# Optimization experiments

Hardware: AMD Instinct MI355X
Metric: run time of the kernel (lower is better)

The kernel has to match this reference:

```python
import jax, jax.numpy as jnp
import numpy as np
from jax import lax

E = 1e-13            # WENO smoothness epsilon
MULT_BIAS = 0.1      # weno5_mult_bias
PADS = (2, 2, 0, 0, 1, 0)


def _conv1d(x, w, b, pad):
    # x: [1, Cin, N], w: [Cout, Cin, K], b: [Cout]
    y = lax.conv_general_dilated(x, w, window_strides=(1,), padding=[(pad, pad)],
                                 dimension_numbers=('NCH', 'OIH', 'NCH'))
    return y + b[None, :, None]


def _cnn(dif, params):
    # inner_nn_weno5: 5 Conv+ELU blocks then Conv+Sigmoid; dif: [N]
    x = dif[None, None, :]
    for i in range(6):
        x = _conv1d(x, params[2 * i], params[2 * i + 1], PADS[i])
        x = jax.nn.elu(x) if i < 5 else jax.nn.sigmoid(x)
    return x[0, 0]  # [N]


def _avg_diff(uu):
    # __get_average_diff: average of left/right forward differences, edges replicated
    d = uu[1:] - uu[:-1]                       # [N-1]
    d_left = jnp.concatenate([d, d[-1:]])      # [N]
    d_right = jnp.concatenate([d[:1], d])      # [N]
    return 0.5 * (d_left + d_right)


def _weno5(uu, params):
    # w5_minus=True, mweno=True, mapped=False, trainable=True
    def fluxes(u):
        um, umm = jnp.roll(u, 1), jnp.roll(u, 2)
        up, upp = jnp.roll(u, -1), jnp.roll(u, -2)
        f0 = (11 * u - 7 * up + 2 * upp) / 6
        f1 = (2 * um + 5 * u - up) / 6
        f2 = (-umm + 5 * um + 2 * u) / 6
        return f0, f1, f2

    def betas(u):
        um, umm = jnp.roll(u, 1), jnp.roll(u, 2)
        up, upp = jnp.roll(u, -1), jnp.roll(u, -2)
        b0 = 13 / 12 * (u - 2 * up + upp) ** 2 + 0.25 * (3 * u - 4 * up + upp) ** 2
        b1 = 13 / 12 * (um - 2 * u + up) ** 2 + 0.25 * (um - up) ** 2
        b2 = 13 / 12 * (umm - 2 * um + u) ** 2 + 0.25 * (umm - 4 * um + 3 * u) ** 2
        return b0, b1, b2

    u_right = jnp.roll(uu, -1)
    fp = fluxes(u_right)
    fn = fluxes(uu)
    bp = list(betas(u_right))
    bn = list(betas(uu))

    # trainable beta correction from the small CNN flux limiter
    bm = _cnn(_avg_diff(uu), params) + MULT_BIAS
    bp = [b * jnp.roll(bm, k - 1) for k, b in enumerate(bp)]
    bn = [b * jnp.roll(bm, k - 1) for k, b in enumerate(bn)]

    ds = (0.1, 0.6, 0.3)

    def omegas(bs):  # mweno=True variant, then normalize
        brs = (bs[2] - bs[0]) ** 2
        om = [d / (E + b) ** 2 * (brs + (E + b) ** 2) for b, d in zip(bs, ds)]
        s = om[0] + om[1] + om[2]
        return [o / s for o in om]

    op = omegas(bp)
    on = omegas(bn)
    fluxp = op[0] * fp[0] + op[1] * fp[1] + op[2] * fp[2]
    fluxn = on[0] * fn[0] + on[1] * fn[1] + on[2] * fn[2]
    return fluxp - fluxn


def setup_inputs() -> dict:
    key = jax.random.key(0)
    ks = jax.random.split(key, 13)
    N = 2097152
    uu = jax.random.normal(ks[0], (N,), dtype=jnp.float32)
    shapes = [(20, 1, 5), (40, 20, 5), (80, 40, 1), (40, 80, 1), (20, 40, 3), (1, 20, 1)]
    inp = {'uu': uu}
    for i, (co, ci, k) in enumerate(shapes):
        fan_in = ci * k
        scale = jnp.float32(1.0 / np.sqrt(fan_in))
        inp[f'w{i + 1}'] = jax.random.normal(ks[2 * i + 1], (co, ci, k), dtype=jnp.float32) * scale
        inp[f'b{i + 1}'] = jax.random.normal(ks[2 * i + 2], (co,), dtype=jnp.float32) * 0.01
    return inp


def reference(uu, w1, b1, w2, b2, w3, b3, w4, b4, w5, b5, w6, b6):
    params = (w1, b1, w2, b2, w3, b3, w4, b4, w5, b5, w6, b6)
    return _weno5(uu, params)
```

## Files before the change

### kernel.cpp

```cpp
#include <hip/hip_runtime.h>
#include <cstdint>

#define N_PTS 2097152
#define MASK  (N_PTS - 1)

constexpr int NPOS = 128;
constexpr int POUT = 116;
constexpr int GOFF = 6;
constexpr int BLK  = 256;
constexpr int NBLK = (N_PTS + POUT - 1) / POUT;

constexpr int ST1 = 40;
constexpr int ST2 = 56;
constexpr int ST3 = 88;
constexpr int ST4 = 56;

constexpr int SLOTA_OFF = 0;
constexpr int SLOTA_SZ  = 22544;
constexpr int SLOTB_OFF = SLOTA_SZ;
constexpr int SLOTB_SZ  = 14576;
constexpr int TAIL_OFF  = SLOTB_OFF + SLOTB_SZ;
constexpr int SMEM_BYTES = TAIL_OFF + 392 * 4;

constexpr int F2 = 0;
constexpr int F3 = 7680;
constexpr int F4 = 12800;
constexpr int F5 = 17408;
constexpr int F1 = 23552;
constexpr int NFRAG2 = 15, NFRAG3 = 10, NFRAG4 = 9, NFRAG5 = 12;
constexpr int NPREP = NFRAG2 + NFRAG3 + NFRAG4 + NFRAG5 + 2;
constexpr int BME_OFF = 65536;

constexpr float L2E = 1.4426950408889634f;
constexpr float LN2 = 0.6931471805599453f;

typedef _Float16 f16x8 __attribute__((ext_vector_type(8)));
typedef _Float16 f16x2 __attribute__((ext_vector_type(2)));
typedef unsigned short u16x8 __attribute__((ext_vector_type(8)));
typedef float f32x4 __attribute__((ext_vector_type(4)));

constexpr unsigned short F16_ONE = 0x3C00;

extern "C" __device__ _Float16 __ocml_exp2_f16(_Float16);

__device__ __forceinline__ float fastrcp(float x) {
#if __has_builtin(__builtin_amdgcn_rcpf)
    return __builtin_amdgcn_rcpf(x);
#else
    return 1.f / x;
#endif
}

__device__ __forceinline__ float fastexp2(float x) {
#if __has_builtin(__builtin_amdgcn_exp2f)
    return __builtin_amdgcn_exp2f(x);
#else
    return __expf(x * LN2);
#endif
}

__device__ __forceinline__ float elu_t(float t) {
    const float e = fastexp2(fminf(t, 0.f));
    return fmaxf(t, fmaf(e, L2E, -L2E));
}

__device__ __forceinline__ unsigned short f2h_rtne(float f) {
    return __builtin_bit_cast(unsigned short, (_Float16)f);
}

__device__ __forceinline__ unsigned int elu2_pk(float t0, float t1) {
    f16x2 h = __builtin_bit_cast(f16x2, __builtin_amdgcn_cvt_pkrtz(t0, t1));
    const f16x2 z = {(_Float16)0.f, (_Float16)0.f};
    f16x2 m = __builtin_elementwise_min(h, z);
    f16x2 e;
    e[0] = __ocml_exp2_f16(m[0]);
    e[1] = __ocml_exp2_f16(m[1]);
    const f16x2 l2e2  = {(_Float16)L2E, (_Float16)L2E};
    const f16x2 nl2e2 = {(_Float16)(-L2E), (_Float16)(-L2E)};
    f16x2 el = __builtin_elementwise_fma(e, l2e2, nl2e2);
    f16x2 r = __builtin_elementwise_max(h, el);
    return __builtin_bit_cast(unsigned int, r);
}

__device__ __forceinline__ unsigned int cvt_pkrtz_u(float lo, float hi) {
    return __builtin_bit_cast(unsigned int, __builtin_amdgcn_cvt_pkrtz(lo, hi));
}

template<int M, int MT, int CI, int KS, int KT>
__device__ __forceinline__ void pack_one(const float* __restrict__ W,
                                         const float* __restrict__ Bias, int biasTap,
                                         unsigned short* __restrict__ dst,
                                         int f, int lane)
{
    const int ks = f % KS;
    const int fi = f / KS;
    const int mt = fi % MT;
    const int t  = fi / MT;
    const int m  = mt * 16 + (lane & 15);
    const int kb = ks * 32 + (lane >> 4) * 8;
    u16x8 v;
    #pragma unroll
    for (int j = 0; j < 8; ++j) {
        const int k = kb + j;
        float val = 0.f;
        if (m < M) {
            if (k < CI)                          val = W[(m * CI + k) * KT + t];
            else if (k == CI && t == biasTap)    val = Bias[m] * L2E;
        }
        v[j] = f2h_rtne(val);
    }
    *(u16x8*)(dst + (f * 64 + lane) * 8) = v;
}

__global__ __launch_bounds__(64) void prep_kernel(
    const float* __restrict__ w1, const float* __restrict__ b1,
    const float* __restrict__ w2, const float* __restrict__ b2,
    const float* __restrict__ w3, const float* __restrict__ b3,
    const float* __restrict__ w4, const float* __restrict__ b4,
    const float* __restrict__ w5, const float* __restrict__ b5,
    unsigned short* __restrict__ frags,
    float* __restrict__ bmE)
{
    const int lane = threadIdx.x;
    const int b = blockIdx.x;
    if (b == 0 && lane < 4) bmE[lane] = 0.f;
    if (b < NFRAG2)
        pack_one<40, 3, 20, 1, 5>(w2, b2, 2, frags + F2, b, lane);
    else if (b < NFRAG2 + NFRAG3)
        pack_one<80, 5, 40, 2, 1>(w3, b3, 0, frags + F3, b - NFRAG2, lane);
    else if (b < NFRAG2 + NFRAG3 + NFRAG4)
        pack_one<40, 3, 80, 3, 1>(w4, b4, 0, frags + F4, b - NFRAG2 - NFRAG3, lane);
    else if (b < NFRAG2 + NFRAG3 + NFRAG4 + NFRAG5)
        pack_one<20, 2, 40, 2, 3>(w5, b5, 1, frags + F5, b - NFRAG2 - NFRAG3 - NFRAG4, lane);
    else {
        const int mt = b - (NPREP - 2);
        const int m  = mt * 16 + (lane & 15);
        const int kb = (lane >> 4) * 8;
        u16x8 v;
        #pragma unroll
        for (int j = 0; j < 8; ++j) {
            const int k = kb + j;
            float val = 0.f;
            if (m < 20) {
                if (k < 5)      val = w1[m * 5 + k] * L2E;
                else if (k == 5) val = b1[m] * L2E;
            }
            v[j] = f2h_rtne(val);
        }
        *(u16x8*)(frags + F1 + (mt * 64 + lane) * 8) = v;
    }
}

template<int NF>
__device__ __forceinline__ void load_A(const unsigned short* __restrict__ Af,
                                       int lane, f16x8* A) {
    #pragma unroll
    for (int f = 0; f < NF; ++f)
        A[f] = __builtin_bit_cast(f16x8, *(const u16x8*)(Af + (f * 64 + lane) * 8));
}

template<int TAPS, int MT, int KS, typename Epi>
__device__ __forceinline__ void gemm_tap(const unsigned short* __restrict__ Af,
                                         const unsigned short* __restrict__ Bbuf,
                                         int SB, f32x4 Z4, Epi epi)
{
    const int lane = threadIdx.x & 63;
    const int wv   = threadIdx.x >> 6;
    const int n15  = lane & 15;
    const int quad = lane >> 4;

    f16x8 A[TAPS * MT * KS];
    load_A<TAPS * MT * KS>(Af, lane, A);

    f16x8 B[2][TAPS][KS];
    #pragma unroll
    for (int nt = 0; nt < 2; ++nt) {
        const int pos = (wv * 2 + nt) * 16 + n15;
        #pragma unroll
        for (int t = 0; t < TAPS; ++t)
            #pragma unroll
            for (int ks = 0; ks < KS; ++ks)
                B[nt][t][ks] = __builtin_bit_cast(f16x8,
                    *(const u16x8*)(Bbuf + (pos + t) * SB + ks * 32 + quad * 8));
    }

    #pragma unroll
    for (int nt = 0; nt < 2; ++nt) {
        const int pos = (wv * 2 + nt) * 16 + n15;
        #pragma unroll
        for (int mt = 0; mt < MT; ++mt) {
            f32x4 acc = __builtin_amdgcn_mfma_f32_16x16x32_f16(
                A[mt * KS], B[nt][0][0], Z4, 0, 0, 0);
            #pragma unroll
            for (int i = 1; i < TAPS * KS; ++i) {
                const int t = i / KS, ks = i - t * KS;
                acc = __builtin_amdgcn_mfma_f32_16x16x32_f16(
                    A[(t * MT + mt) * KS + ks], B[nt][t][ks], acc, 0, 0, 0);
            }
            epi(mt, pos, acc);
        }
    }
}

__device__ __forceinline__ float weno_math(float um2, float um1, float u0,
                                           float up1, float up2, float up3,
                                           float bmm, float bm0, float bmp)
{
    const float c1312 = 13.f / 12.f;
    const float s6 = 1.f / 6.f;

    const float f0p = (11.f * up1 - 7.f * up2 + 2.f * up3) * s6;
    const float f1p = (2.f * u0 + 5.f * up1 - up2) * s6;
    const float f2p = (-um1 + 5.f * u0 + 2.f * up1) * s6;
    const float f0n = (11.f * u0 - 7.f * up1 + 2.f * up2) * s6;
    const float f1n = (2.f * um1 + 5.f * u0 - up1) * s6;
    const float f2n = (-um2 + 5.f * um1 + 2.f * u0) * s6;

    float t0, t1;
    t0 = up1 - 2.f * up2 + up3;  t1 = 3.f * up1 - 4.f * up2 + up3;
    float bp0 = c1312 * t0 * t0 + 0.25f * t1 * t1;
    t0 = u0 - 2.f * up1 + up2;   t1 = u0 - up2;
    float bp1 = c1312 * t0 * t0 + 0.25f * t1 * t1;
    t0 = um1 - 2.f * u0 + up1;   t1 = um1 - 4.f * u0 + 3.f * up1;
    float bp2 = c1312 * t0 * t0 + 0.25f * t1 * t1;
    t0 = u0 - 2.f * up1 + up2;   t1 = 3.f * u0 - 4.f * up1 + up2;
    float bn0 = c1312 * t0 * t0 + 0.25f * t1 * t1;
    t0 = um1 - 2.f * u0 + up1;   t1 = um1 - up1;
    float bn1 = c1312 * t0 * t0 + 0.25f * t1 * t1;
    t0 = um2 - 2.f * um1 + u0;   t1 = um2 - 4.f * um1 + 3.f * u0;
    float bn2 = c1312 * t0 * t0 + 0.25f * t1 * t1;

    bp0 *= bmp; bp1 *= bm0; bp2 *= bmm;
    bn0 *= bmp; bn1 *= bm0; bn2 *= bmm;

    const float E = 1e-13f;
    float brs, e, r0, r1, r2, o0, o1, o2;

    brs = bp2 - bp0; brs *= brs;
    e = E + bp0; e *= e; r0 = fastrcp(e);
    e = E + bp1; e *= e; r1 = fastrcp(e);
    e = E + bp2; e *= e; r2 = fastrcp(e);
    o0 = 0.1f * fmaf(brs, r0, 1.f);
    o1 = 0.6f * fmaf(brs, r1, 1.f);
    o2 = 0.3f * fmaf(brs, r2, 1.f);
    const float fluxp = (o0 * f0p + o1 * f1p + o2 * f2p) * fastrcp(o0 + o1 + o2);

    brs = bn2 - bn0; brs *= brs;
    e = E + bn0; e *= e; r0 = fastrcp(e);
    e = E + bn1; e *= e; r1 = fastrcp(e);
    e = E + bn2; e *= e; r2 = fastrcp(e);
    o0 = 0.1f * fmaf(brs, r0, 1.f);
    o1 = 0.6f * fmaf(brs, r1, 1.f);
    o2 = 0.3f * fmaf(brs, r2, 1.f);
    const float fluxn = (o0 * f0n + o1 * f1n + o2 * f2n) * fastrcp(o0 + o1 + o2);

    return fluxp - fluxn;
}

__global__ __launch_bounds__(BLK, 4) void cnn_weno_kernel(
    const float* __restrict__ u,
    const float* __restrict__ w6, const float* __restrict__ b6,
    const unsigned short* __restrict__ frags,
    float* __restrict__ bmE,
    float* __restrict__ out)
{
    if (blockIdx.x == NBLK) {
        if (threadIdx.x == 0) {
            float b0, b1, b2, b3;
            for (;;) {
                b0 = __hip_atomic_load(&bmE[0], __ATOMIC_ACQUIRE, __HIP_MEMORY_SCOPE_AGENT);
                b1 = __hip_atomic_load(&bmE[1], __ATOMIC_ACQUIRE, __HIP_MEMORY_SCOPE_AGENT);
                b2 = __hip_atomic_load(&bmE[2], __ATOMIC_ACQUIRE, __HIP_MEMORY_SCOPE_AGENT);
                b3 = __hip_atomic_load(&bmE[3], __ATOMIC_ACQUIRE, __HIP_MEMORY_SCOPE_AGENT);
                if (b0 != 0.f && b1 != 0.f && b2 != 0.f && b3 != 0.f) break;
                __builtin_amdgcn_s_sleep(2);
            }
            out[0] = weno_math(u[N_PTS - 2], u[N_PTS - 1], u[0],
                               u[1], u[2], u[3], b3, b0, b1);
            out[N_PTS - 1] = weno_math(u[N_PTS - 3], u[N_PTS - 2], u[N_PTS - 1],
                                       u[0], u[1], u[2], b2, b3, b0);
        }
        return;
    }

    extern __shared__ char smem[];
    unsigned short* act1 = (unsigned short*)(smem + SLOTA_OFF);
    unsigned short* act3 = (unsigned short*)(smem + SLOTA_OFF);
    unsigned short* act2 = (unsigned short*)(smem + SLOTB_OFF);
    unsigned short* act4 = (unsigned short*)(smem + SLOTB_OFF);
    float* sdif = (float*)(smem + TAIL_OFF);
    float* sw6  = sdif + 132;
    float* sb6  = sw6 + 20;
    float* sbm  = sb6 + 1;
    float* su   = sbm + 118;

    const int tid  = threadIdx.x;
    const int lane = tid & 63;
    const int wv   = tid >> 6;
    const int n15  = lane & 15;
    const int quad = lane >> 4;
    const int i0   = blockIdx.x * POUT;
    const bool edge = (blockIdx.x == 0) || (blockIdx.x >= NBLK - 1);

    const f32x4 Z4 = {0.f, 0.f, 0.f, 0.f};

    {
        const u16x8 z8 = {0, 0, 0, 0, 0, 0, 0, 0};
        for (int r = tid; r < 130; r += BLK)
            *(u16x8*)(act2 + r * ST2 + 48) = z8;
        if (tid < 20)       *(u16x8*)(act1 + 128 * ST1 + tid * 8) = z8;
        else if (tid == 20) *(u16x8*)(act2 + 128 * ST2) = z8;
        else if (tid == 21) *(u16x8*)(act3 + 128 * ST3) = z8;
        else if (tid < 28)  *(u16x8*)(act4 + 129 * ST4 + (tid - 22) * 8) = z8;
        else if (tid == 28) *(u16x8*)(act4 + 130 * ST4) = z8;
    }
    if (!edge) {
        for (int d = tid; d < 132; d += BLK) {
            const int g = i0 - 10 + d;
            sdif[d] = 0.5f * (u[g + 1] - u[g - 1]);
        }
        for (int j = tid; j < 121; j += BLK)
            su[j] = u[i0 - 2 + j];
    } else {
        for (int d = tid; d < 132; d += BLK) {
            const int g = i0 - 10 + d;
            float v = 0.f;
            if (g >= 0 && g < N_PTS) {
                if (g == 0)              v = u[1] - u[0];
                else if (g == N_PTS - 1) v = u[N_PTS - 1] - u[N_PTS - 2];
                else                     v = 0.5f * (u[g + 1] - u[g - 1]);
            }
            sdif[d] = v;
        }
        for (int j = tid; j < 121; j += BLK)
            su[j] = u[(i0 - 2 + j) & MASK];
    }
    if (tid < 20)       sw6[tid] = w6[tid] * LN2;
    else if (tid == 20) sb6[0] = b6[0];
    __syncthreads();

    {
        f16x8 A1[2];
        load_A<2>(frags + F1, lane, A1);
        float s[2][5];
        #pragma unroll
        for (int nt = 0; nt < 2; ++nt) {
            const int pos = (wv * 2 + nt) * 16 + n15;
            #pragma unroll
            for (int j = 0; j < 5; ++j)
                s[nt][j] = sdif[pos + j];
        }
        #pragma unroll
        for (int nt = 0; nt < 2; ++nt) {
            const int pos = (wv * 2 + nt) * 16 + n15;
            uint4 bd;
            bd.x = cvt_pkrtz_u(s[nt][0], s[nt][1]);
            bd.y = cvt_pkrtz_u(s[nt][2], s[nt][3]);
            bd.z = cvt_pkrtz_u(s[nt][4], 1.0f);
            bd.w = 0u;
            const f16x8 B = __builtin_bit_cast(f16x8, bd);
            const f32x4 a0 = __builtin_amdgcn_mfma_f32_16x16x32_f16(A1[0], B, Z4, 0, 0, 0);
            const f32x4 a1 = __builtin_amdgcn_mfma_f32_16x16x32_f16(A1[1], B, Z4, 0, 0, 0);
            bool oor = false;
            if (edge) {
                const int g = i0 + pos - 8;
                oor = ((unsigned)g >= (unsigned)N_PTS);
            }
            {
                uint2 w;
                w.x = elu2_pk(a0[0], a0[1]); w.y = elu2_pk(a0[2], a0[3]);
                if (oor) { w.x = 0u; w.y = 0u; }
                *(uint2*)(act1 + pos * ST1 + quad * 4) = w;
            }
            {
                uint2 w;
                if (quad == 0) {
                    w.x = elu2_pk(a1[0], a1[1]); w.y = elu2_pk(a1[2], a1[3]);
                    if (oor) { w.x = 0u; w.y = 0u; }
                } else if (quad == 1) {
                    w.x = (unsigned)F16_ONE; w.y = 0u;
                } else {
                    w.x = 0u; w.y = 0u;
                }
                *(uint2*)(act1 + pos * ST1 + 16 + quad * 4) = w;
            }
        }
    }
    __syncthreads();

    gemm_tap<5, 3, 1>(frags + F2, act1, ST1, Z4,
        [&](int mt, int pos, f32x4 acc) {
            const int ch0 = mt * 16 + quad * 4;
            unsigned short* dst = act2 + pos * ST2 + ch0;
            if (mt < 2 || quad < 2) {
                uint2 w;
                w.x = elu2_pk(acc[0], acc[1]); w.y = elu2_pk(acc[2], acc[3]);
                if (edge) {
                    const int g = i0 - GOFF + pos;
                    if ((unsigned)g >= (unsigned)N_PTS) { w.x = 0u; w.y = 0u; }
                }
                *(uint2*)dst = w;
            } else {
                uint2 w; w.x = (quad == 2) ? (unsigned)F16_ONE : 0u; w.y = 0u;
                *(uint2*)dst = w;
            }
        });
    __syncthreads();

    {
        u16x8 v = {F16_ONE, 0, 0, 0, 0, 0, 0, 0};
        for (int r = tid; r < 128; r += BLK)
            *(u16x8*)(act3 + r * ST3 + 80) = v;
    }
    gemm_tap<1, 5, 2>(frags + F3, act2, ST2, Z4,
        [&](int mt, int pos, f32x4 acc) {
            const int ch0 = mt * 16 + quad * 4;
            uint2 w;
            w.x = elu2_pk(acc[0], acc[1]); w.y = elu2_pk(acc[2], acc[3]);
            if (edge) {
                const int g = i0 - GOFF + pos;
                if ((unsigned)g >= (unsigned)N_PTS) { w.x = 0u; w.y = 0u; }
            }
            *(uint2*)(act3 + pos * ST3 + ch0) = w;
        });
    __syncthreads();

    gemm_tap<1, 3, 3>(frags + F4, act3, ST3, Z4,
        [&](int mt, int pos, f32x4 acc) {
            const int ch0 = mt * 16 + quad * 4;
            unsigned short* dst = act4 + (pos + 1) * ST4 + ch0;
            if (mt < 2 || quad < 2) {
                uint2 w;
                w.x = elu2_pk(acc[0], acc[1]); w.y = elu2_pk(acc[2], acc[3]);
                if (edge) {
                    const int g = i0 - GOFF + pos;
                    if ((unsigned)g >= (unsigned)N_PTS) { w.x = 0u; w.y = 0u; }
                }
                *(uint2*)dst = w;
            } else {
                uint2 w; w.x = (quad == 2) ? (unsigned)F16_ONE : 0u; w.y = 0u;
                *(uint2*)dst = w;
            }
        });
    __syncthreads();

    {
        f16x8 A5[12];
        load_A<12>(frags + F5, lane, A5);
        #pragma unroll
        for (int nt = 0; nt < 2; ++nt) {
            const int pos = (wv * 2 + nt) * 16 + n15;
            f16x8 B[3][2];
            #pragma unroll
            for (int t = 0; t < 3; ++t)
                #pragma unroll
                for (int ks = 0; ks < 2; ++ks)
                    B[t][ks] = __builtin_bit_cast(f16x8,
                        *(const u16x8*)(act4 + (pos + t) * ST4 + ks * 32 + quad * 8));
            f32x4 a0 = __builtin_amdgcn_mfma_f32_16x16x32_f16(A5[0], B[0][0], Z4, 0, 0, 0);
            f32x4 a1 = __builtin_amdgcn_mfma_f32_16x16x32_f16(A5[2], B[0][0], Z4, 0, 0, 0);
            #pragma unroll
            for (int i = 1; i < 6; ++i) {
                const int t = i >> 1, ks = i & 1;
                a0 = __builtin_amdgcn_mfma_f32_16x16x32_f16(
                    A5[(t * 2 + 0) * 2 + ks], B[t][ks], a0, 0, 0, 0);
                a1 = __builtin_amdgcn_mfma_f32_16x16x32_f16(
                    A5[(t * 2 + 1) * 2 + ks], B[t][ks], a1, 0, 0, 0);
            }
            float partial = 0.f;
            const int c0 = quad * 4;
            #pragma unroll
            for (int r = 0; r < 4; ++r)
                partial += sw6[c0 + r] * elu_t(a0[r]);
            if (quad == 0) {
                #pragma unroll
                for (int r = 0; r < 4; ++r)
                    partial += sw6[16 + r] * elu_t(a1[r]);
            }
            partial += __shfl_xor(partial, 16, 64);
            partial += __shfl_xor(partial, 32, 64);
            if (quad == 0) {
                const float bmv = fastrcp(1.f + __expf(-(partial + sb6[0]))) + 0.1f;
                if (pos >= 5 && pos < 123) sbm[pos - 5] = bmv;
                if (edge) {
                    const int g = i0 - GOFF + pos;
                    if (blockIdx.x == 0) {
                        if (g == 0)
                            __hip_atomic_store(&bmE[0], bmv, __ATOMIC_RELEASE, __HIP_MEMORY_SCOPE_AGENT);
                        else if (g == 1)
                            __hip_atomic_store(&bmE[1], bmv, __ATOMIC_RELEASE, __HIP_MEMORY_SCOPE_AGENT);
                    }
                    if (blockIdx.x == NBLK - 1) {
                        if (g == N_PTS - 2)
                            __hip_atomic_store(&bmE[2], bmv, __ATOMIC_RELEASE, __HIP_MEMORY_SCOPE_AGENT);
                        else if (g == N_PTS - 1)
                            __hip_atomic_store(&bmE[3], bmv, __ATOMIC_RELEASE, __HIP_MEMORY_SCOPE_AGENT);
                    }
                }
            }
        }
    }
    __syncthreads();

    if (tid < POUT) {
        const int g = i0 + tid;
        if (g < N_PTS && g != 0 && g != N_PTS - 1) {
            out[g] = weno_math(su[tid], su[tid + 1], su[tid + 2],
                               su[tid + 3], su[tid + 4], su[tid + 5],
                               sbm[tid], sbm[tid + 1], sbm[tid + 2]);
        }
    }
}

extern "C" void kernel_launch(void* const* d_in, const int* in_sizes, int n_in,
                              void* d_out, int out_size, void* d_ws, size_t ws_size,
                              hipStream_t stream) {
    const float* u  = (const float*)d_in[0];
    const float* w1 = (const float*)d_in[1];
    const float* b1 = (const float*)d_in[2];
    const float* w2 = (const float*)d_in[3];
    const float* b2 = (const float*)d_in[4];
    const float* w3 = (const float*)d_in[5];
    const float* b3 = (const float*)d_in[6];
    const float* w4 = (const float*)d_in[7];
    const float* b4 = (const float*)d_in[8];
    const float* w5 = (const float*)d_in[9];
    const float* b5 = (const float*)d_in[10];
    const float* w6 = (const float*)d_in[11];
    const float* b6 = (const float*)d_in[12];

    unsigned short* frags = (unsigned short*)d_ws;
    float* bmE = (float*)((char*)d_ws + BME_OFF);

    (void)hipFuncSetAttribute((const void*)cnn_weno_kernel,
                              hipFuncAttributeMaxDynamicSharedMemorySize,
                              SMEM_BYTES);

    prep_kernel<<<NPREP, 64, 0, stream>>>(w1, b1, w2, b2, w3, b3, w4, b4, w5, b5,
                                          frags, bmE);
    cnn_weno_kernel<<<NBLK + 1, BLK, SMEM_BYTES, stream>>>(u, w6, b6, frags, bmE,
                                                           (float*)d_out);
}
```

Measured before the change: 250.6 us.

## Fuse conv3 and conv4 in registers, dropping act3 shared buffer

Layer 3's MFMA outputs are packed to f16 in registers and reused directly as the B operand for layer 4. This works because the accumulator layout matches the B-fragment layout once w4 is pre-permuted in the prep kernel. This removes the act3 shared-memory round trip and one __syncthreads, and shrinks LDS enough to raise launch bounds to 5 blocks per CU. The cost is extra live registers for the packed intermediate, plus a permuted weight layout that must exactly match the MFMA lane mapping.

```diff
diff --git a/kernel.cpp b/kernel.cpp
--- a/kernel.cpp
+++ b/kernel.cpp
@@ -12,13 +12,12 @@
 
 constexpr int ST1 = 40;
 constexpr int ST2 = 56;
-constexpr int ST3 = 88;
 constexpr int ST4 = 56;
 
 constexpr int SLOTA_OFF = 0;
-constexpr int SLOTA_SZ  = 22544;
+constexpr int SLOTA_SZ  = 14576;
 constexpr int SLOTB_OFF = SLOTA_SZ;
-constexpr int SLOTB_SZ  = 14576;
+constexpr int SLOTB_SZ  = 14352;
 constexpr int TAIL_OFF  = SLOTB_OFF + SLOTB_SZ;
 constexpr int SMEM_BYTES = TAIL_OFF + 392 * 4;
 
@@ -128,8 +127,31 @@
         pack_one<40, 3, 20, 1, 5>(w2, b2, 2, frags + F2, b, lane);
     else if (b < NFRAG2 + NFRAG3)
         pack_one<80, 5, 40, 2, 1>(w3, b3, 0, frags + F3, b - NFRAG2, lane);
-    else if (b < NFRAG2 + NFRAG3 + NFRAG4)
-        pack_one<40, 3, 80, 3, 1>(w4, b4, 0, frags + F4, b - NFRAG2 - NFRAG3, lane);
+    else if (b < NFRAG2 + NFRAG3 + NFRAG4) {
+        const int f  = b - NFRAG2 - NFRAG3;
+        const int ks = f % 3;
+        const int mt = f / 3;
+        const int m  = mt * 16 + (lane & 15);
+        const int q  = lane >> 4;
+        u16x8 v;
+        #pragma unroll
+        for (int j = 0; j < 8; ++j) {
+            float val = 0.f;
+            if (m < 40) {
+                if (ks < 2) {
+                    const int ch = ks * 32 + ((j >> 2) << 4) + q * 4 + (j & 3);
+                    val = w4[m * 80 + ch];
+                } else if (j < 4) {
+                    const int ch = 64 + q * 4 + j;
+                    val = w4[m * 80 + ch];
+                } else if (j == 4 && q == 0) {
+                    val = b4[m] * L2E;
+                }
+            }
+            v[j] = f2h_rtne(val);
+        }
+        *(u16x8*)(frags + F4 + (f * 64 + lane) * 8) = v;
+    }
     else if (b < NFRAG2 + NFRAG3 + NFRAG4 + NFRAG5)
         pack_one<20, 2, 40, 2, 3>(w5, b5, 1, frags + F5, b - NFRAG2 - NFRAG3 - NFRAG4, lane);
     else {
@@ -257,7 +279,7 @@
     return fluxp - fluxn;
 }
 
-__global__ __launch_bounds__(BLK, 4) void cnn_weno_kernel(
+__global__ __launch_bounds__(BLK, 5) void cnn_weno_kernel(
     const float* __restrict__ u,
     const float* __restrict__ w6, const float* __restrict__ b6,
     const unsigned short* __restrict__ frags,
@@ -285,9 +307,8 @@
 
     extern __shared__ char smem[];
     unsigned short* act1 = (unsigned short*)(smem + SLOTA_OFF);
-    unsigned short* act3 = (unsigned short*)(smem + SLOTA_OFF);
+    unsigned short* act4 = (unsigned short*)(smem + SLOTA_OFF);
     unsigned short* act2 = (unsigned short*)(smem + SLOTB_OFF);
-    unsigned short* act4 = (unsigned short*)(smem + SLOTB_OFF);
     float* sdif = (float*)(smem + TAIL_OFF);
     float* sw6  = sdif + 132;
     float* sb6  = sw6 + 20;
@@ -307,12 +328,14 @@
     {
         const u16x8 z8 = {0, 0, 0, 0, 0, 0, 0, 0};
         for (int r = tid; r < 130; r += BLK)
+            *(u16x8*)(act4 + r * ST4 + 48) = z8;
+        for (int r = tid; r < 128; r += BLK)
             *(u16x8*)(act2 + r * ST2 + 48) = z8;
         if (tid < 20)       *(u16x8*)(act1 + 128 * ST1 + tid * 8) = z8;
         else if (tid == 20) *(u16x8*)(act2 + 128 * ST2) = z8;
-        else if (tid == 21) *(u16x8*)(act3 + 128 * ST3) = z8;
-        else if (tid < 28)  *(u16x8*)(act4 + 129 * ST4 + (tid - 22) * 8) = z8;
-        else if (tid == 28) *(u16x8*)(act4 + 130 * ST4) = z8;
+        else if (tid < 27)  *(u16x8*)(act4 + 129 * ST4 + (tid - 21) * 8) = z8;
+        else if (tid == 27) *(u16x8*)(act4 + 130 * ST4) = z8;
+        else if (tid < 34)  *(u16x8*)(act4 + (tid - 28) * 8) = z8;
     }
     if (!edge) {
         for (int d = tid; d < 132; d += BLK) {
@@ -408,40 +431,73 @@
     __syncthreads();
 
     {
-        u16x8 v = {F16_ONE, 0, 0, 0, 0, 0, 0, 0};
-        for (int r = tid; r < 128; r += BLK)
-            *(u16x8*)(act3 + r * ST3 + 80) = v;
-    }
-    gemm_tap<1, 5, 2>(frags + F3, act2, ST2, Z4,
-        [&](int mt, int pos, f32x4 acc) {
-            const int ch0 = mt * 16 + quad * 4;
-            uint2 w;
-            w.x = elu2_pk(acc[0], acc[1]); w.y = elu2_pk(acc[2], acc[3]);
-            if (edge) {
-                const int g = i0 - GOFF + pos;
-                if ((unsigned)g >= (unsigned)N_PTS) { w.x = 0u; w.y = 0u; }
-            }
-            *(uint2*)(act3 + pos * ST3 + ch0) = w;
-        });
-    __syncthreads();
-
-    gemm_tap<1, 3, 3>(frags + F4, act3, ST3, Z4,
-        [&](int mt, int pos, f32x4 acc) {
-            const int ch0 = mt * 16 + quad * 4;
-            unsigned short* dst = act4 + (pos + 1) * ST4 + ch0;
-            if (mt < 2 || quad < 2) {
-                uint2 w;
-                w.x = elu2_pk(acc[0], acc[1]); w.y = elu2_pk(acc[2], acc[3]);
-                if (edge) {
-                    const int g = i0 - GOFF + pos;
-                    if ((unsigned)g >= (unsigned)N_PTS) { w.x = 0u; w.y = 0u; }
+        unsigned int p[2][5][2];
+        {
+            f16x8 A3[10];
+            load_A<10>(frags + F3, lane, A3);
+            f16x8 B3[2][2];
+            #pragma unroll
+            for (int nt = 0; nt < 2; ++nt) {
+                const int pos = (wv * 2 + nt) * 16 + n15;
+                #pragma unroll
+                for (int ks = 0; ks < 2; ++ks)
+                    B3[nt][ks] = __builtin_bit_cast(f16x8,
+                        *(const u16x8*)(act2 + pos * ST2 + ks * 32 + quad * 8));
+            }
+            #pragma unroll
+            for (int nt = 0; nt < 2; ++nt) {
+                #pragma unroll
+                for (int mt = 0; mt < 5; ++mt) {
+                    f32x4 acc = __builtin_amdgcn_mfma_f32_16x16x32_f16(
+                        A3[mt * 2 + 0], B3[nt][0], Z4, 0, 0, 0);
+                    acc = __builtin_amdgcn_mfma_f32_16x16x32_f16(
+                        A3[mt * 2 + 1], B3[nt][1], acc, 0, 0, 0);
+                    p[nt][mt][0] = elu2_pk(acc[0], acc[1]);
+                    p[nt][mt][1] = elu2_pk(acc[2], acc[3]);
                 }
-                *(uint2*)dst = w;
-            } else {
-                uint2 w; w.x = (quad == 2) ? (unsigned)F16_ONE : 0u; w.y = 0u;
-                *(uint2*)dst = w;
-            }
-        });
+            }
+        }
+        {
+            f16x8 A4[9];
+            load_A<9>(frags + F4, lane, A4);
+            const unsigned int biasw = (quad == 0) ? (unsigned)F16_ONE : 0u;
+            #pragma unroll
+            for (int nt = 0; nt < 2; ++nt) {
+                const int pos = (wv * 2 + nt) * 16 + n15;
+                uint4 w0, w1, w2;
+                w0.x = p[nt][0][0]; w0.y = p[nt][0][1]; w0.z = p[nt][1][0]; w0.w = p[nt][1][1];
+                w1.x = p[nt][2][0]; w1.y = p[nt][2][1]; w1.z = p[nt][3][0]; w1.w = p[nt][3][1];
+                w2.x = p[nt][4][0]; w2.y = p[nt][4][1]; w2.z = biasw;       w2.w = 0u;
+                f16x8 B4[3];
+                B4[0] = __builtin_bit_cast(f16x8, w0);
+                B4[1] = __builtin_bit_cast(f16x8, w1);
+                B4[2] = __builtin_bit_cast(f16x8, w2);
+                #pragma unroll
+                for (int mt = 0; mt < 3; ++mt) {
+                    f32x4 acc = __builtin_amdgcn_mfma_f32_16x16x32_f16(
+                        A4[mt * 3 + 0], B4[0], Z4, 0, 0, 0);
+                    acc = __builtin_amdgcn_mfma_f32_16x16x32_f16(
+                        A4[mt * 3 + 1], B4[1], acc, 0, 0, 0);
+                    acc = __builtin_amdgcn_mfma_f32_16x16x32_f16(
+                        A4[mt * 3 + 2], B4[2], acc, 0, 0, 0);
+                    const int ch0 = mt * 16 + quad * 4;
+                    unsigned short* dst = act4 + (pos + 1) * ST4 + ch0;
+                    if (mt < 2 || quad < 2) {
+                        uint2 w;
+                        w.x = elu2_pk(acc[0], acc[1]); w.y = elu2_pk(acc[2], acc[3]);
+                        if (edge) {
+                            const int g = i0 - GOFF + pos;
+                            if ((unsigned)g >= (unsigned)N_PTS) { w.x = 0u; w.y = 0u; }
+                        }
+                        *(uint2*)dst = w;
+                    } else {
+                        uint2 w; w.x = (quad == 2) ? (unsigned)F16_ONE : 0u; w.y = 0u;
+                        *(uint2*)dst = w;
+                    }
+                }
+            }
+        }
+    }
     __syncthreads();
 
     {
```

Measured after the change: 244.3 us. 1.03x faster.
